# Kernel optimization log

Hardware: AMD Instinct MI355X
Metric: run time of the kernel (lower is better)

The kernel has to match this reference:

```python
import jax, jax.numpy as jnp
import numpy as np

RENORM_PERIOD = 256
MAX_NORM = 100.0


def setup_inputs() -> dict:
    key = jax.random.key(0)
    ks = jax.random.split(key, 9)
    B, S, G, D, N = 4, 2048, 8, 128, 64
    return {
        "x_r": jax.random.normal(ks[0], (B, S, G, D), jnp.float32),
        "x_i": jax.random.normal(ks[1], (B, S, G, D), jnp.float32),
        "log_A_mag": jax.random.uniform(ks[2], (G, N), jnp.float32) * 0.5 + 0.5,
        "A_phase": jax.random.normal(ks[3], (G, N), jnp.float32) * 0.1,
        "Bw_r": jax.random.normal(ks[4], (N, D), jnp.float32) / np.sqrt(D),
        "Bw_i": jax.random.normal(ks[5], (N, D), jnp.float32) / np.sqrt(D),
        "Cw_r": jax.random.normal(ks[6], (D, N), jnp.float32) / np.sqrt(N),
        "Cw_i": jax.random.normal(ks[7], (D, N), jnp.float32) / np.sqrt(N),
        "dt_w": jax.random.normal(ks[8], (2, 2 * D), jnp.float32) * 0.02,
        "dt_b": jnp.zeros((2,), jnp.float32),
    }


def reference(x_r, x_i, log_A_mag, A_phase, Bw_r, Bw_i, Cw_r, Cw_i, dt_w, dt_b):
    B, S, G, D = x_r.shape
    N = Bw_r.shape[0]
    # dt: input-dependent step magnitude / phase scale, clamped
    x_cat = jnp.concatenate([x_r, x_i], axis=-1)            # [B,S,G,2D]
    dt = jnp.clip(jnp.exp(jnp.einsum('bsgd,od->bsgo', x_cat, dt_w) + dt_b), 1e-4, 2.0)
    dt_mag = dt[..., 0:1]                                    # [B,S,G,1]
    dt_phase = dt[..., 1:2]
    # A_bar in polar form, |A| = exp(-softplus(log_A_mag)*dt_mag) < 1
    neg_log_A = -jax.nn.softplus(log_A_mag)[None, None]      # [1,1,G,N]
    A_mag = jnp.exp(dt_mag * neg_log_A)                      # [B,S,G,N]
    A_ang = dt_phase * A_phase[None, None]
    A_r = A_mag * jnp.cos(A_ang)
    A_i = A_mag * jnp.sin(A_ang)
    # Bx = (B_proj @ x) * dt_mag, complex linear
    Bx_r = (jnp.einsum('bsgd,nd->bsgn', x_r, Bw_r) - jnp.einsum('bsgd,nd->bsgn', x_i, Bw_i)) * dt_mag
    Bx_i = (jnp.einsum('bsgd,nd->bsgn', x_r, Bw_i) + jnp.einsum('bsgd,nd->bsgn', x_i, Bw_r)) * dt_mag

    def step(carry, inp):
        h_r, h_i = carry
        ar, ai, br, bi, t = inp
        nh_r = ar * h_r - ai * h_i + br
        nh_i = ar * h_i + ai * h_r + bi
        renorm = ((t + 1) % RENORM_PERIOD) == 0
        norm = jnp.sqrt(nh_r * nh_r + nh_i * nh_i + 1e-8)
        scale = jnp.minimum(norm, MAX_NORM) / norm
        nh_r = jnp.where(renorm, nh_r * scale, nh_r)
        nh_i = jnp.where(renorm, nh_i * scale, nh_i)
        return (nh_r, nh_i), (nh_r, nh_i)

    h0 = (jnp.zeros((B, G, N), jnp.float32), jnp.zeros((B, G, N), jnp.float32))
    xs = (jnp.moveaxis(A_r, 1, 0), jnp.moveaxis(A_i, 1, 0),
          jnp.moveaxis(Bx_r, 1, 0), jnp.moveaxis(Bx_i, 1, 0),
          jnp.arange(S))
    _, (all_h_r, all_h_i) = jax.lax.scan(step, h0, xs)       # [S,B,G,N]
    all_h_r = jnp.moveaxis(all_h_r, 0, 1)                    # [B,S,G,N]
    all_h_i = jnp.moveaxis(all_h_i, 0, 1)
    # y = C_proj(h), complex linear N -> D
    y_r = jnp.einsum('bsgn,dn->bsgd', all_h_r, Cw_r) - jnp.einsum('bsgn,dn->bsgd', all_h_i, Cw_i)
    y_i = jnp.einsum('bsgn,dn->bsgd', all_h_r, Cw_i) + jnp.einsum('bsgn,dn->bsgd', all_h_i, Cw_r)
    return jnp.stack([y_r, y_i], axis=0)                     # [2,B,S,G,D]
```

## Files before the change

kernel.cpp:

```cpp
#include <hip/hip_runtime.h>
#include <math.h>

#define B_ 4
#define S_ 2048
#define G_ 8
#define D_ 128
#define N_ 64
#define ROWS (B_*S_*G_)
#define CH 64
#define CLEN 32
#define NCHAIN (B_*G_*N_)
#define YOFF (ROWS*D_)

typedef short bf16x8 __attribute__((ext_vector_type(8)));
typedef float f32x4  __attribute__((ext_vector_type(4)));
#define MFMA16(a,b,c) __builtin_amdgcn_mfma_f32_16x16x32_bf16(a,b,c,0,0,0)

__device__ __forceinline__ unsigned short bf16_rtne(float f) {
    unsigned u = __float_as_uint(f);
    unsigned r = (u + 0x7FFFu + ((u >> 16) & 1u)) >> 16;
    return (unsigned short)r;
}
__device__ __forceinline__ void split_bf16(float f, unsigned short &hi, unsigned short &lo) {
    hi = bf16_rtne(f);
    float hif = __uint_as_float(((unsigned)hi) << 16);
    lo = bf16_rtne(f - hif);
}
__device__ __forceinline__ void split4(float4 v, uint2 &hi2, uint2 &lo2) {
    unsigned short h0,h1,h2,h3,l0,l1,l2,l3;
    split_bf16(v.x,h0,l0); split_bf16(v.y,h1,l1);
    split_bf16(v.z,h2,l2); split_bf16(v.w,h3,l3);
    hi2 = make_uint2((unsigned)h0 | ((unsigned)h1<<16), (unsigned)h2 | ((unsigned)h3<<16));
    lo2 = make_uint2((unsigned)l0 | ((unsigned)l1<<16), (unsigned)l2 | ((unsigned)l3<<16));
}
__device__ __forceinline__ float dot4(float4 a, float4 b) {
    return fmaf(a.x,b.x, fmaf(a.y,b.y, fmaf(a.z,b.z, a.w*b.w)));
}

__global__ __launch_bounds__(256) void k_prep(
    const float* __restrict__ bwr, const float* __restrict__ bwi,
    const float* __restrict__ cwr, const float* __restrict__ cwi,
    unsigned short* __restrict__ wbhi, unsigned short* __restrict__ wblo,
    unsigned short* __restrict__ wchi)
{
    int tid = blockIdx.x * 256 + threadIdx.x;
    if (tid < 4096) {
        int f = tid;
        int lane = f & 63, ks = (f >> 6) & 7, nt = (f >> 9) & 1, w = f >> 10;
        int l15 = lane & 15, quad = lane >> 4;
        int n = w * 32 + nt * 16 + l15;
        int k0 = ks * 32 + quad * 8;
        const float* src; float sgn = 1.f;
        if (n < 64) {
            if (k0 < 128) src = bwr + n * 128 + k0;
            else        { src = bwi + n * 128 + (k0 - 128); sgn = -1.f; }
        } else {
            if (k0 < 128) src = bwi + (n - 64) * 128 + k0;
            else          src = bwr + (n - 64) * 128 + (k0 - 128);
        }
        float4 v0 = *(const float4*)src;
        float4 v1 = *(const float4*)(src + 4);
        float vv[8] = {v0.x,v0.y,v0.z,v0.w,v1.x,v1.y,v1.z,v1.w};
        unsigned short h[8], l[8];
        #pragma unroll
        for (int j = 0; j < 8; j++) split_bf16(vv[j] * sgn, h[j], l[j]);
        #pragma unroll
        for (int j = 0; j < 8; j++) { wbhi[f*8+j] = h[j]; wblo[f*8+j] = l[j]; }
    } else {
        int f = tid - 4096;
        int lane = f & 63, ks = (f >> 6) & 3, nt = (f >> 8) & 3, w = f >> 10;
        int l15 = lane & 15, quad = lane >> 4;
        int n = w * 64 + nt * 16 + l15;
        int d = (n < 128) ? n : (n - 128);
        int k0 = ks * 32 + quad * 8;
        const float* src; float sgn = 1.f;
        if (n < 128) {
            if (k0 < 64) src = cwr + d * 64 + k0;
            else       { src = cwi + d * 64 + (k0 - 64); sgn = -1.f; }
        } else {
            if (k0 < 64) src = cwi + d * 64 + k0;
            else         src = cwr + d * 64 + (k0 - 64);
        }
        float4 v0 = *(const float4*)src;
        float4 v1 = *(const float4*)(src + 4);
        float vv[8] = {v0.x,v0.y,v0.z,v0.w,v1.x,v1.y,v1.z,v1.w};
        unsigned short h[8], l[8];
        #pragma unroll
        for (int j = 0; j < 8; j++) split_bf16(vv[j] * sgn, h[j], l[j]);
        #pragma unroll
        for (int j = 0; j < 8; j++) wchi[f*8+j] = h[j];
    }
}

#define LDK1 280
__global__ __launch_bounds__(256, 4) void k_g1(
    const float* __restrict__ xr, const float* __restrict__ xi,
    const float* __restrict__ dtw, const float* __restrict__ dtb,
    const float* __restrict__ logAm, const float* __restrict__ Aph,
    const unsigned short* __restrict__ wbhi, const unsigned short* __restrict__ wblo,
    float* __restrict__ bxr, float* __restrict__ bxi,
    float* __restrict__ dt_mag, float* __restrict__ dt_ph,
    float4* __restrict__ trans)
{
    __shared__ __align__(16) unsigned short Ahi[32 * LDK1];
    __shared__ __align__(16) unsigned short Alo[32 * LDK1];
    __shared__ float dms[32], dps[32];
    __shared__ float4 comb[64];
    float* bxs = (float*)Ahi;
    const int t = threadIdx.x;
    const int lane = t & 63, w = t >> 6;
    const int l15 = lane & 15, quad = lane >> 4;
    const int bg = blockIdx.x >> 6, c = blockIdx.x & 63;
    const int g = bg & 7, b = bg >> 3;

    const int kq = t & 31, k4 = kq * 4;
    float4 w0r = *(const float4*)(dtw + k4);
    float4 w0i = *(const float4*)(dtw + 128 + k4);
    float4 w1r = *(const float4*)(dtw + 256 + k4);
    float4 w1i = *(const float4*)(dtw + 384 + k4);
    float b0 = dtb[0], b1 = dtb[1];
    float nla = -logf(1.0f + __expf(logAm[g * N_ + lane]));
    float aph = Aph[g * N_ + lane];

    const int s0 = c * CLEN;
    const float* xrb = xr + ((size_t)(b * S_ + s0) * G_ + g) * 128;
    const float* xib = xi + ((size_t)(b * S_ + s0) * G_ + g) * 128;

    float pm[4], pp[4];
    #pragma unroll
    for (int i = 0; i < 4; i++) {
        int f = t + 256 * i;
        int m = f >> 5, kk = f & 31;
        float4 a  = ((const float4*)(xrb + m * 1024))[kk];
        float4 bb = ((const float4*)(xib + m * 1024))[kk];
        uint2 h2, l2;
        split4(a, h2, l2);
        *(uint2*)&Ahi[m * LDK1 + kk * 4] = h2;
        *(uint2*)&Alo[m * LDK1 + kk * 4] = l2;
        split4(bb, h2, l2);
        *(uint2*)&Ahi[m * LDK1 + 128 + kk * 4] = h2;
        *(uint2*)&Alo[m * LDK1 + 128 + kk * 4] = l2;
        pm[i] = dot4(a, w0r) + dot4(bb, w0i);
        pp[i] = dot4(a, w1r) + dot4(bb, w1i);
    }
    #pragma unroll
    for (int i = 0; i < 4; i++) {
        float vm = pm[i], vp = pp[i];
        #pragma unroll
        for (int msk = 16; msk >= 1; msk >>= 1) {
            vm += __shfl_xor(vm, msk);
            vp += __shfl_xor(vp, msk);
        }
        if ((t & 31) == 0) {
            int m = (t >> 5) + 8 * i;
            float dm = fminf(fmaxf(__expf(vm + b0), 1e-4f), 2.0f);
            float dp = fminf(fmaxf(__expf(vp + b1), 1e-4f), 2.0f);
            dms[m] = dm; dps[m] = dp;
            int row = (b * S_ + s0 + m) * G_ + g;
            dt_mag[row] = dm; dt_ph[row] = dp;
        }
    }
    __syncthreads();

    f32x4 acc[2][2];
    #pragma unroll
    for (int a = 0; a < 2; a++)
        #pragma unroll
        for (int bq = 0; bq < 2; bq++)
            acc[a][bq] = (f32x4){0.f, 0.f, 0.f, 0.f};
    #pragma unroll
    for (int ks = 0; ks < 8; ks++) {
        bf16x8 wh0 = ((const bf16x8*)wbhi)[((w * 2 + 0) * 8 + ks) * 64 + lane];
        bf16x8 wl0 = ((const bf16x8*)wblo)[((w * 2 + 0) * 8 + ks) * 64 + lane];
        bf16x8 wh1 = ((const bf16x8*)wbhi)[((w * 2 + 1) * 8 + ks) * 64 + lane];
        bf16x8 wl1 = ((const bf16x8*)wblo)[((w * 2 + 1) * 8 + ks) * 64 + lane];
        #pragma unroll
        for (int ms = 0; ms < 2; ms++) {
            int arow = (ms * 16 + l15) * LDK1 + quad * 8;
            bf16x8 ah = *(const bf16x8*)&Ahi[arow + ks * 32];
            bf16x8 al = *(const bf16x8*)&Alo[arow + ks * 32];
            acc[ms][0] = MFMA16(al, wh0, acc[ms][0]);
            acc[ms][0] = MFMA16(ah, wl0, acc[ms][0]);
            acc[ms][0] = MFMA16(ah, wh0, acc[ms][0]);
            acc[ms][1] = MFMA16(al, wh1, acc[ms][1]);
            acc[ms][1] = MFMA16(ah, wl1, acc[ms][1]);
            acc[ms][1] = MFMA16(ah, wh1, acc[ms][1]);
        }
    }
    __syncthreads();

    #pragma unroll
    for (int ms = 0; ms < 2; ms++)
        #pragma unroll
        for (int nt = 0; nt < 2; nt++) {
            int n = w * 32 + nt * 16 + l15;
            float* dstg = (n < 64) ? bxr : bxi;
            int nn = n & 63;
            #pragma unroll
            for (int r = 0; r < 4; r++) {
                int m = ms * 16 + quad * 4 + r;
                float v = acc[ms][nt][r] * dms[m];
                dstg[((b * S_ + s0 + m) * G_ + g) * 64 + nn] = v;
                bxs[m * 132 + n] = v;
            }
        }
    __syncthreads();

    float Ar = 1.f, Ai = 0.f, Br = 0.f, Bi = 0.f;
    if (w < 2) {
        int base = w * 16;
        #pragma unroll
        for (int tt = 0; tt < 16; tt++) {
            int m = base + tt;
            float dm = dms[m], dp = dps[m];
            float am  = __expf(dm * nla);
            float ang = dp * aph;
            float cr = am * __cosf(ang), ci = am * __sinf(ang);
            float vr = bxs[m * 132 + lane], vi = bxs[m * 132 + 64 + lane];
            float nAr = cr * Ar - ci * Ai;
            float nAi = cr * Ai + ci * Ar;
            float nBr = cr * Br - ci * Bi + vr;
            float nBi = cr * Bi + ci * Br + vi;
            Ar = nAr; Ai = nAi; Br = nBr; Bi = nBi;
        }
        if (w == 0) comb[lane] = make_float4(Ar, Ai, Br, Bi);
    }
    __syncthreads();
    if (w == 1) {
        float4 c0 = comb[lane];
        float fAr = Ar * c0.x - Ai * c0.y;
        float fAi = Ar * c0.y + Ai * c0.x;
        float fBr = Ar * c0.z - Ai * c0.w + Br;
        float fBi = Ar * c0.w + Ai * c0.z + Bi;
        trans[(bg * CH + c) * 64 + lane] = make_float4(fAr, fAi, fBr, fBi);
    }
}

__global__ __launch_bounds__(256) void k_scanB2(const float4* __restrict__ trans,
    float2* __restrict__ hstart)
{
    int w = threadIdx.x >> 6, lane = threadIdx.x & 63;
    int W = blockIdx.x * 4 + w;
    int bg = W >> 3;
    int n  = ((W & 7) << 3) + (lane & 7);
    int j  = lane >> 3;
    float pAr[8], pAi[8], pBr[8], pBi[8];
    float Ar = 1.f, Ai = 0.f, Br = 0.f, Bi = 0.f;
    const float4* tp = trans + (bg * CH + j * 8) * 64 + n;
    #pragma unroll
    for (int k = 0; k < 8; k++) {
        pAr[k] = Ar; pAi[k] = Ai; pBr[k] = Br; pBi[k] = Bi;
        float4 T = tp[k * 64];
        float nAr = T.x * Ar - T.y * Ai;
        float nAi = T.x * Ai + T.y * Ar;
        float nBr = T.x * Br - T.y * Bi + T.z;
        float nBi = T.x * Bi + T.y * Br + T.w;
        Ar = nAr; Ai = nAi; Br = nBr; Bi = nBi;
    }
    float hr = 0.f, hi = 0.f, mhr = 0.f, mhi = 0.f;
    #pragma unroll
    for (int j2 = 0; j2 < 8; j2++) {
        if (j2 == j) { mhr = hr; mhi = hi; }
        int src = j2 * 8 + (lane & 7);
        float sAr = __shfl(Ar, src), sAi = __shfl(Ai, src);
        float sBr = __shfl(Br, src), sBi = __shfl(Bi, src);
        float nr = sAr * hr - sAi * hi + sBr;
        float ni = sAr * hi + sAi * hr + sBi;
        float nrm = sqrtf(nr * nr + ni * ni + 1e-8f);
        float sc = fminf(nrm, 100.f) / nrm;
        hr = nr * sc; hi = ni * sc;
    }
    float2* hp = hstart + (bg * CH + j * 8) * 64 + n;
    #pragma unroll
    for (int k = 0; k < 8; k++) {
        float hsr = pAr[k] * mhr - pAi[k] * mhi + pBr[k];
        float hsi = pAr[k] * mhi + pAi[k] * mhr + pBi[k];
        hp[k * 64] = make_float2(hsr, hsi);
    }
}

#define LDK2 152
__global__ __launch_bounds__(256, 4) void k_sg2(
    const float* __restrict__ bxr, const float* __restrict__ bxi,
    const float* __restrict__ dt_mag, const float* __restrict__ dt_ph,
    const float* __restrict__ logAm, const float* __restrict__ Aph,
    const float2* __restrict__ hstart,
    const unsigned short* __restrict__ wchi,
    float* __restrict__ out)
{
    __shared__ __align__(16) unsigned short Ahi[64 * LDK2];
    __shared__ __align__(16) unsigned short Alo[64 * LDK2];
    const int t = threadIdx.x;
    const int lane = t & 63, w = t >> 6;
    const int l15 = lane & 15, quad = lane >> 4;
    const int bg = blockIdx.x >> 5, cp = blockIdx.x & 31;
    const int g = bg & 7, b = bg >> 3;

    if (w < 2) {
        const int n = lane;
        const int c = cp * 2 + w;
        float nla = -logf(1.0f + __expf(logAm[g * N_ + n]));
        float aph = Aph[g * N_ + n];
        float2 h0 = hstart[(bg * CH + c) * 64 + n];
        float hr = h0.x, hi = h0.y;
        const bool rn = ((c & 7) == 7);
        const int rowbase = (b * S_ + c * CLEN) * G_ + g;
        #pragma unroll 8
        for (int tt = 0; tt < CLEN; tt++) {
            int row = rowbase + tt * G_;
            float dm = dt_mag[row], dp = dt_ph[row];
            float am  = __expf(dm * nla);
            float ang = dp * aph;
            float cr = am * __cosf(ang), ci = am * __sinf(ang);
            float vr = bxr[row * N_ + n], vi = bxi[row * N_ + n];
            float nr = cr * hr - ci * hi + vr;
            float ni = cr * hi + ci * hr + vi;
            if (rn && tt == CLEN - 1) {
                float nrm = sqrtf(nr * nr + ni * ni + 1e-8f);
                float scale = fminf(nrm, 100.0f) / nrm;
                nr *= scale; ni *= scale;
            }
            hr = nr; hi = ni;
            int m = w * 32 + tt;
            unsigned short hh, hl;
            split_bf16(hr, hh, hl);
            Ahi[m * LDK2 + n] = hh;  Alo[m * LDK2 + n] = hl;
            split_bf16(hi, hh, hl);
            Ahi[m * LDK2 + 64 + n] = hh;  Alo[m * LDK2 + 64 + n] = hl;
        }
    }
    __syncthreads();

    f32x4 acc[4][4];
    #pragma unroll
    for (int a = 0; a < 4; a++)
        #pragma unroll
        for (int bq = 0; bq < 4; bq++)
            acc[a][bq] = (f32x4){0.f, 0.f, 0.f, 0.f};
    #pragma unroll
    for (int ks = 0; ks < 4; ks++) {
        bf16x8 wc0 = ((const bf16x8*)wchi)[((w * 4 + 0) * 4 + ks) * 64 + lane];
        bf16x8 wc1 = ((const bf16x8*)wchi)[((w * 4 + 1) * 4 + ks) * 64 + lane];
        bf16x8 wc2 = ((const bf16x8*)wchi)[((w * 4 + 2) * 4 + ks) * 64 + lane];
        bf16x8 wc3 = ((const bf16x8*)wchi)[((w * 4 + 3) * 4 + ks) * 64 + lane];
        #pragma unroll
        for (int ms = 0; ms < 4; ms++) {
            int arow = (ms * 16 + l15) * LDK2 + quad * 8;
            bf16x8 ah = *(const bf16x8*)&Ahi[arow + ks * 32];
            bf16x8 al = *(const bf16x8*)&Alo[arow + ks * 32];
            acc[ms][0] = MFMA16(al, wc0, acc[ms][0]);
            acc[ms][0] = MFMA16(ah, wc0, acc[ms][0]);
            acc[ms][1] = MFMA16(al, wc1, acc[ms][1]);
            acc[ms][1] = MFMA16(ah, wc1, acc[ms][1]);
            acc[ms][2] = MFMA16(al, wc2, acc[ms][2]);
            acc[ms][2] = MFMA16(ah, wc2, acc[ms][2]);
            acc[ms][3] = MFMA16(al, wc3, acc[ms][3]);
            acc[ms][3] = MFMA16(ah, wc3, acc[ms][3]);
        }
    }
    #pragma unroll
    for (int ms = 0; ms < 4; ms++)
        #pragma unroll
        for (int nt = 0; nt < 4; nt++) {
            int nn = w * 64 + nt * 16 + l15;
            float* dst = (nn < 128) ? (out + nn) : (out + YOFF + (nn - 128));
            #pragma unroll
            for (int r = 0; r < 4; r++) {
                int m_local = ms * 16 + quad * 4 + r;
                int cc = m_local >> 5, tt2 = m_local & 31;
                int srow = (b * S_ + (cp * 2 + cc) * CLEN + tt2) * G_ + g;
                dst[srow * 128] = acc[ms][nt][r];
            }
        }
}

extern "C" void kernel_launch(void* const* d_in, const int* in_sizes, int n_in,
                              void* d_out, int out_size, void* d_ws, size_t ws_size,
                              hipStream_t stream) {
    (void)in_sizes; (void)n_in; (void)out_size; (void)ws_size;
    const float* xr    = (const float*)d_in[0];
    const float* xi    = (const float*)d_in[1];
    const float* logAm = (const float*)d_in[2];
    const float* Aph   = (const float*)d_in[3];
    const float* bwr   = (const float*)d_in[4];
    const float* bwi   = (const float*)d_in[5];
    const float* cwr   = (const float*)d_in[6];
    const float* cwi   = (const float*)d_in[7];
    const float* dtw   = (const float*)d_in[8];
    const float* dtb   = (const float*)d_in[9];
    float* out = (float*)d_out;
    float* ws  = (float*)d_ws;

    float*  dt_mag = ws;
    float*  dt_ph  = ws + 65536;
    float*  bxr    = ws + 131072;
    float*  bxi    = bxr + 4194304;
    float4* trans  = (float4*)(ws + 8519680);
    float2* hstart = (float2*)(ws + 9043968);
    unsigned short* wbhi = (unsigned short*)(ws + 9306112);
    unsigned short* wblo = wbhi + 32768;
    unsigned short* wchi = wblo + 32768;

    hipLaunchKernelGGL(k_prep,   dim3(32), dim3(256), 0, stream,
                       bwr, bwi, cwr, cwi, wbhi, wblo, wchi);
    hipLaunchKernelGGL(k_g1,     dim3((B_ * G_) * 64), dim3(256), 0, stream,
                       xr, xi, dtw, dtb, logAm, Aph, wbhi, wblo,
                       bxr, bxi, dt_mag, dt_ph, trans);
    hipLaunchKernelGGL(k_scanB2, dim3(64), dim3(256), 0, stream,
                       trans, hstart);
    hipLaunchKernelGGL(k_sg2,    dim3((B_ * G_) * 32), dim3(256), 0, stream,
                       bxr, bxi, dt_mag, dt_ph, logAm, Aph, hstart, wchi, out);
}
```

Baseline: 160.3 us.

## Chunk-contiguous intermediates, packed bf16 split, one chunk per sg2 block

Intermediates (dt, Bx) are now stored chunk-contiguously so the serial scan in k_sg2 reads consecutive addresses. The bf16 hi/lo split switches to the hardware packed conversion instruction. The C-weight K dimension is interleaved real/imag so h can be stored as packed pairs. k_sg2 now handles one chunk per block with a single scanning wave and doubles the grid with a higher occupancy hint. The aim is to shorten the serial scan latency and raise parallelism, at the cost of more blocks and more repeated loads of the C weights.

```diff
diff --git a/kernel.cpp b/kernel.cpp
--- a/kernel.cpp
+++ b/kernel.cpp
@@ -26,12 +26,20 @@
     float hif = __uint_as_float(((unsigned)hi) << 16);
     lo = bf16_rtne(f - hif);
 }
-__device__ __forceinline__ void split4(float4 v, uint2 &hi2, uint2 &lo2) {
-    unsigned short h0,h1,h2,h3,l0,l1,l2,l3;
-    split_bf16(v.x,h0,l0); split_bf16(v.y,h1,l1);
-    split_bf16(v.z,h2,l2); split_bf16(v.w,h3,l3);
-    hi2 = make_uint2((unsigned)h0 | ((unsigned)h1<<16), (unsigned)h2 | ((unsigned)h3<<16));
-    lo2 = make_uint2((unsigned)l0 | ((unsigned)l1<<16), (unsigned)l2 | ((unsigned)l3<<16));
+__device__ __forceinline__ unsigned pk_bf16(float a, float b) {
+    unsigned r;
+    asm("v_cvt_pk_bf16_f32 %0, %1, %2" : "=v"(r) : "v"(a), "v"(b));
+    return r;
+}
+__device__ __forceinline__ void split4_pk(float4 v, uint2 &hi2, uint2 &lo2) {
+    unsigned p0 = pk_bf16(v.x, v.y);
+    unsigned p1 = pk_bf16(v.z, v.w);
+    float r0 = v.x - __uint_as_float(p0 << 16);
+    float r1 = v.y - __uint_as_float(p0 & 0xFFFF0000u);
+    float r2 = v.z - __uint_as_float(p1 << 16);
+    float r3 = v.w - __uint_as_float(p1 & 0xFFFF0000u);
+    hi2 = make_uint2(p0, p1);
+    lo2 = make_uint2(pk_bf16(r0, r1), pk_bf16(r2, r3));
 }
 __device__ __forceinline__ float dot4(float4 a, float4 b) {
     return fmaf(a.x,b.x, fmaf(a.y,b.y, fmaf(a.z,b.z, a.w*b.w)));
@@ -73,20 +81,16 @@
         int n = w * 64 + nt * 16 + l15;
         int d = (n < 128) ? n : (n - 128);
         int k0 = ks * 32 + quad * 8;
-        const float* src; float sgn = 1.f;
-        if (n < 128) {
-            if (k0 < 64) src = cwr + d * 64 + k0;
-            else       { src = cwi + d * 64 + (k0 - 64); sgn = -1.f; }
-        } else {
-            if (k0 < 64) src = cwi + d * 64 + k0;
-            else         src = cwr + d * 64 + (k0 - 64);
-        }
-        float4 v0 = *(const float4*)src;
-        float4 v1 = *(const float4*)(src + 4);
-        float vv[8] = {v0.x,v0.y,v0.z,v0.w,v1.x,v1.y,v1.z,v1.w};
-        unsigned short h[8], l[8];
-        #pragma unroll
-        for (int j = 0; j < 8; j++) split_bf16(vv[j] * sgn, h[j], l[j]);
+        unsigned short h[8];
+        #pragma unroll
+        for (int j = 0; j < 8; j++) {
+            int k = k0 + j, col = k >> 1;
+            float val;
+            if (n < 128) val = (k & 1) ? -cwi[d * 64 + col] : cwr[d * 64 + col];
+            else         val = (k & 1) ?  cwr[d * 64 + col] : cwi[d * 64 + col];
+            unsigned short hh, hl; split_bf16(val, hh, hl);
+            h[j] = hh;
+        }
         #pragma unroll
         for (int j = 0; j < 8; j++) wchi[f*8+j] = h[j];
     }
@@ -112,6 +116,7 @@
     const int l15 = lane & 15, quad = lane >> 4;
     const int bg = blockIdx.x >> 6, c = blockIdx.x & 63;
     const int g = bg & 7, b = bg >> 3;
+    const int crow = (bg * CH + c) * CLEN;
 
     const int kq = t & 31, k4 = kq * 4;
     float4 w0r = *(const float4*)(dtw + k4);
@@ -134,10 +139,10 @@
         float4 a  = ((const float4*)(xrb + m * 1024))[kk];
         float4 bb = ((const float4*)(xib + m * 1024))[kk];
         uint2 h2, l2;
-        split4(a, h2, l2);
+        split4_pk(a, h2, l2);
         *(uint2*)&Ahi[m * LDK1 + kk * 4] = h2;
         *(uint2*)&Alo[m * LDK1 + kk * 4] = l2;
-        split4(bb, h2, l2);
+        split4_pk(bb, h2, l2);
         *(uint2*)&Ahi[m * LDK1 + 128 + kk * 4] = h2;
         *(uint2*)&Alo[m * LDK1 + 128 + kk * 4] = l2;
         pm[i] = dot4(a, w0r) + dot4(bb, w0i);
@@ -156,8 +161,7 @@
             float dm = fminf(fmaxf(__expf(vm + b0), 1e-4f), 2.0f);
             float dp = fminf(fmaxf(__expf(vp + b1), 1e-4f), 2.0f);
             dms[m] = dm; dps[m] = dp;
-            int row = (b * S_ + s0 + m) * G_ + g;
-            dt_mag[row] = dm; dt_ph[row] = dp;
+            dt_mag[crow + m] = dm; dt_ph[crow + m] = dp;
         }
     }
     __syncthreads();
@@ -200,7 +204,7 @@
             for (int r = 0; r < 4; r++) {
                 int m = ms * 16 + quad * 4 + r;
                 float v = acc[ms][nt][r] * dms[m];
-                dstg[((b * S_ + s0 + m) * G_ + g) * 64 + nn] = v;
+                dstg[(crow + m) * 64 + nn] = v;
                 bxs[m * 132 + n] = v;
             }
         }
@@ -280,7 +284,7 @@
 }
 
 #define LDK2 152
-__global__ __launch_bounds__(256, 4) void k_sg2(
+__global__ __launch_bounds__(256, 6) void k_sg2(
     const float* __restrict__ bxr, const float* __restrict__ bxi,
     const float* __restrict__ dt_mag, const float* __restrict__ dt_ph,
     const float* __restrict__ logAm, const float* __restrict__ Aph,
@@ -288,31 +292,30 @@
     const unsigned short* __restrict__ wchi,
     float* __restrict__ out)
 {
-    __shared__ __align__(16) unsigned short Ahi[64 * LDK2];
-    __shared__ __align__(16) unsigned short Alo[64 * LDK2];
+    __shared__ __align__(16) unsigned short Ahi[32 * LDK2];
+    __shared__ __align__(16) unsigned short Alo[32 * LDK2];
     const int t = threadIdx.x;
     const int lane = t & 63, w = t >> 6;
     const int l15 = lane & 15, quad = lane >> 4;
-    const int bg = blockIdx.x >> 5, cp = blockIdx.x & 31;
+    const int bg = blockIdx.x >> 6, c = blockIdx.x & 63;
     const int g = bg & 7, b = bg >> 3;
 
-    if (w < 2) {
+    if (w == 0) {
         const int n = lane;
-        const int c = cp * 2 + w;
         float nla = -logf(1.0f + __expf(logAm[g * N_ + n]));
         float aph = Aph[g * N_ + n];
         float2 h0 = hstart[(bg * CH + c) * 64 + n];
         float hr = h0.x, hi = h0.y;
         const bool rn = ((c & 7) == 7);
-        const int rowbase = (b * S_ + c * CLEN) * G_ + g;
+        const int base = (bg * CH + c) * CLEN;
         #pragma unroll 8
         for (int tt = 0; tt < CLEN; tt++) {
-            int row = rowbase + tt * G_;
-            float dm = dt_mag[row], dp = dt_ph[row];
+            float dm = dt_mag[base + tt], dp = dt_ph[base + tt];
             float am  = __expf(dm * nla);
             float ang = dp * aph;
             float cr = am * __cosf(ang), ci = am * __sinf(ang);
-            float vr = bxr[row * N_ + n], vi = bxi[row * N_ + n];
+            float vr = bxr[(base + tt) * 64 + n];
+            float vi = bxi[(base + tt) * 64 + n];
             float nr = cr * hr - ci * hi + vr;
             float ni = cr * hi + ci * hr + vi;
             if (rn && tt == CLEN - 1) {
@@ -321,19 +324,19 @@
                 nr *= scale; ni *= scale;
             }
             hr = nr; hi = ni;
-            int m = w * 32 + tt;
-            unsigned short hh, hl;
-            split_bf16(hr, hh, hl);
-            Ahi[m * LDK2 + n] = hh;  Alo[m * LDK2 + n] = hl;
-            split_bf16(hi, hh, hl);
-            Ahi[m * LDK2 + 64 + n] = hh;  Alo[m * LDK2 + 64 + n] = hl;
+            unsigned hp = pk_bf16(hr, hi);
+            float rr = hr - __uint_as_float(hp << 16);
+            float ri = hi - __uint_as_float(hp & 0xFFFF0000u);
+            unsigned lp = pk_bf16(rr, ri);
+            *(unsigned*)&Ahi[tt * LDK2 + 2 * n] = hp;
+            *(unsigned*)&Alo[tt * LDK2 + 2 * n] = lp;
         }
     }
     __syncthreads();
 
-    f32x4 acc[4][4];
-    #pragma unroll
-    for (int a = 0; a < 4; a++)
+    f32x4 acc[2][4];
+    #pragma unroll
+    for (int a = 0; a < 2; a++)
         #pragma unroll
         for (int bq = 0; bq < 4; bq++)
             acc[a][bq] = (f32x4){0.f, 0.f, 0.f, 0.f};
@@ -344,7 +347,7 @@
         bf16x8 wc2 = ((const bf16x8*)wchi)[((w * 4 + 2) * 4 + ks) * 64 + lane];
         bf16x8 wc3 = ((const bf16x8*)wchi)[((w * 4 + 3) * 4 + ks) * 64 + lane];
         #pragma unroll
-        for (int ms = 0; ms < 4; ms++) {
+        for (int ms = 0; ms < 2; ms++) {
             int arow = (ms * 16 + l15) * LDK2 + quad * 8;
             bf16x8 ah = *(const bf16x8*)&Ahi[arow + ks * 32];
             bf16x8 al = *(const bf16x8*)&Alo[arow + ks * 32];
@@ -359,16 +362,15 @@
         }
     }
     #pragma unroll
-    for (int ms = 0; ms < 4; ms++)
+    for (int ms = 0; ms < 2; ms++)
         #pragma unroll
         for (int nt = 0; nt < 4; nt++) {
             int nn = w * 64 + nt * 16 + l15;
             float* dst = (nn < 128) ? (out + nn) : (out + YOFF + (nn - 128));
             #pragma unroll
             for (int r = 0; r < 4; r++) {
-                int m_local = ms * 16 + quad * 4 + r;
-                int cc = m_local >> 5, tt2 = m_local & 31;
-                int srow = (b * S_ + (cp * 2 + cc) * CLEN + tt2) * G_ + g;
+                int tt2 = ms * 16 + quad * 4 + r;
+                int srow = (b * S_ + c * CLEN + tt2) * G_ + g;
                 dst[srow * 128] = acc[ms][nt][r];
             }
         }
@@ -408,6 +410,6 @@
                        bxr, bxi, dt_mag, dt_ph, trans);
     hipLaunchKernelGGL(k_scanB2, dim3(64), dim3(256), 0, stream,
                        trans, hstart);
-    hipLaunchKernelGGL(k_sg2,    dim3((B_ * G_) * 32), dim3(256), 0, stream,
+    hipLaunchKernelGGL(k_sg2,    dim3((B_ * G_) * 64), dim3(256), 0, stream,
                        bxr, bxi, dt_mag, dt_ph, logAm, Aph, hstart, wchi, out);
 }
```

New measurement: 165.2 us. +3.0%, slower.
